# Optimization experiments

Hardware: AMD Instinct MI355X
Metric: run time of the kernel (lower is better)

Reference implementation:

```python
import jax, jax.numpy as jnp
import numpy as np

NUM_HEADS = 16
HEAD_DIM = 64  # d_out // num_heads = 1024 // 16


def setup_inputs() -> dict:
    key = jax.random.key(0)
    ks = jax.random.split(key, 9)
    B, S, D = 2, 2048, 1024
    scale = 0.02
    return {
        "x": jax.random.normal(ks[0], (B, S, D), jnp.float32),
        "Wq": jax.random.normal(ks[1], (D, D), jnp.float32) * scale,
        "bq": jax.random.normal(ks[2], (D,), jnp.float32) * scale,
        "Wk": jax.random.normal(ks[3], (D, D), jnp.float32) * scale,
        "bk": jax.random.normal(ks[4], (D,), jnp.float32) * scale,
        "Wv": jax.random.normal(ks[5], (D, D), jnp.float32) * scale,
        "bv": jax.random.normal(ks[6], (D,), jnp.float32) * scale,
        "Wo": jax.random.normal(ks[7], (D, D), jnp.float32) * scale,
        "bo": jax.random.normal(ks[8], (D,), jnp.float32) * scale,
    }


def reference(x, Wq, bq, Wk, bk, Wv, bv, Wo, bo):
    B, S, D = x.shape
    H, Dh = NUM_HEADS, HEAD_DIM
    # QKV projections (torch Linear: x @ W.T + b; here W stored as [d_in, d_out])
    q = (x @ Wq + bq).reshape(B, S, H, Dh).transpose(0, 2, 1, 3)  # [B,H,S,Dh]
    k = (x @ Wk + bk).reshape(B, S, H, Dh).transpose(0, 2, 1, 3)
    v = (x @ Wv + bv).reshape(B, S, H, Dh).transpose(0, 2, 1, 3)
    scores = jnp.einsum("bhqd,bhkd->bhqk", q, k)
    # causal mask applied before scaling (as in source; -inf unaffected by scale)
    causal = jnp.tril(jnp.ones((S, S), dtype=bool))
    scores = jnp.where(causal, scores, -jnp.inf) / jnp.sqrt(jnp.float32(Dh))
    attn = jax.nn.softmax(scores, axis=-1)  # dropout=0.0 (eval)
    ctx = jnp.einsum("bhqk,bhkd->bhqd", attn, v)  # [B,H,S,Dh]
    ctx = ctx.transpose(0, 2, 1, 3).reshape(B, S, D)
    return ctx @ Wo + bo
```

## Files before the change

### kernel.cpp

```cpp
#include <hip/hip_runtime.h>
#include <math.h>


#define H_  16
#define DH_ 64
#define D_  1024
#define S_  2048
#define B_  2

typedef __attribute__((ext_vector_type(8))) short short8;
typedef __attribute__((ext_vector_type(4))) float f32x4;

__device__ __forceinline__ unsigned short f2bf(float f) {
    union { float f; unsigned int u; } v; v.f = f;
    unsigned int r = (v.u + 0x7fffu + ((v.u >> 16) & 1u)) >> 16;
    return (unsigned short)r;
}

__device__ __forceinline__ void gload_lds16(const void* g, void* l) {
    __builtin_amdgcn_global_load_lds(
        (const __attribute__((address_space(1))) void*)g,
        (__attribute__((address_space(3))) void*)l, 16, 0, 0);
}

__global__ __launch_bounds__(256) void cvt_x_k(const float* __restrict__ x,
                                               unsigned short* __restrict__ xb)
{
    int i = (blockIdx.x * 256 + threadIdx.x) * 8;
    float4 a = *(const float4*)&x[i];
    float4 b = *(const float4*)&x[i + 4];
    uint4 o;
    o.x = f2bf(a.x) | ((unsigned)f2bf(a.y) << 16);
    o.y = f2bf(a.z) | ((unsigned)f2bf(a.w) << 16);
    o.z = f2bf(b.x) | ((unsigned)f2bf(b.y) << 16);
    o.w = f2bf(b.z) | ((unsigned)f2bf(b.w) << 16);
    *(uint4*)&xb[i] = o;
}

__global__ __launch_bounds__(256) void tr_w_k(
    const float* __restrict__ W0, const float* __restrict__ W1,
    const float* __restrict__ W2, const float* __restrict__ W3,
    unsigned short* __restrict__ wt)
{
    const float* W = W0;
    if (blockIdx.z == 1) W = W1; else if (blockIdx.z == 2) W = W2;
    else if (blockIdx.z == 3) W = W3;
    unsigned short* out = wt + (size_t)blockIdx.z * 1048576;

    __shared__ float t[64][65];
    const int k0 = blockIdx.x * 64, n0 = blockIdx.y * 64;
    const int r = threadIdx.x >> 4, c4 = (threadIdx.x & 15) * 4;

    #pragma unroll
    for (int p = 0; p < 4; ++p) {
        float4 v = *(const float4*)&W[(size_t)(k0 + r + 16 * p) * D_ + n0 + c4];
        t[r + 16 * p][c4 + 0] = v.x; t[r + 16 * p][c4 + 1] = v.y;
        t[r + 16 * p][c4 + 2] = v.z; t[r + 16 * p][c4 + 3] = v.w;
    }
    __syncthreads();
    #pragma unroll
    for (int p = 0; p < 4; ++p) {
        int nn = r + 16 * p;
        uint2 o;
        o.x = f2bf(t[c4 + 0][nn]) | ((unsigned)f2bf(t[c4 + 1][nn]) << 16);
        o.y = f2bf(t[c4 + 2][nn]) | ((unsigned)f2bf(t[c4 + 3][nn]) << 16);
        *(uint2*)&out[(size_t)(n0 + nn) * D_ + k0 + c4] = o;
    }
}

template<int QKV>
__global__ __launch_bounds__(256) void gemm_bf16(
    const unsigned short* __restrict__ Ab,
    const unsigned short* __restrict__ Wt,
    const float* __restrict__ b0, const float* __restrict__ b1,
    const float* __restrict__ b2,
    void* __restrict__ o0, void* __restrict__ o1, void* __restrict__ o2)
{
    const unsigned short* W = Wt;
    const float* bias = b0;
    int z = 0;
    if (QKV) {
        z = blockIdx.z;
        W = Wt + (size_t)z * 1048576;
        if (z == 1) bias = b1; else if (z == 2) bias = b2;
    }
    const int n0 = blockIdx.x * 128, j0 = blockIdx.y * 128;
    const int tid = threadIdx.x;
    const int lane = tid & 63;
    const int wq = tid >> 6, wm = wq >> 1, wn = wq & 1;
    const int lr = lane & 15, lk = lane >> 4;

    __shared__ __align__(16) char smem[32768];

    f32x4 acc[4][4] = {};

    for (int k0 = 0; k0 < D_; k0 += 64) {
        __syncthreads();
        #pragma unroll
        for (int c = 0; c < 4; ++c) {
            int u = c * 256 + tid;
            int r = u >> 3, sp = u & 7, sl = sp ^ (r & 7);
            gload_lds16(&Ab[(size_t)(n0 + r) * D_ + k0 + sl * 8], &smem[u * 16]);
        }
        #pragma unroll
        for (int c = 0; c < 4; ++c) {
            int u = c * 256 + tid;
            int r = u >> 3, sp = u & 7, sl = sp ^ (r & 7);
            gload_lds16(&W[(size_t)(j0 + r) * D_ + k0 + sl * 8],
                        &smem[16384 + u * 16]);
        }
        __syncthreads();
        #pragma unroll
        for (int kc = 0; kc < 2; ++kc) {
            short8 a[4], b[4];
            #pragma unroll
            for (int m = 0; m < 4; ++m) {
                int row = wm * 64 + m * 16 + lr;
                int sp = (kc * 4 + lk) ^ (row & 7);
                a[m] = *(const short8*)&smem[row * 128 + sp * 16];
            }
            #pragma unroll
            for (int n = 0; n < 4; ++n) {
                int row = wn * 64 + n * 16 + lr;
                int sp = (kc * 4 + lk) ^ (row & 7);
                b[n] = *(const short8*)&smem[16384 + row * 128 + sp * 16];
            }
            #pragma unroll
            for (int m = 0; m < 4; ++m)
                #pragma unroll
                for (int n = 0; n < 4; ++n)
                    acc[m][n] = __builtin_amdgcn_mfma_f32_16x16x32_bf16(
                        a[m], b[n], acc[m][n], 0, 0, 0);
        }
    }

    float bn[4];
    #pragma unroll
    for (int n = 0; n < 4; ++n) bn[n] = bias[j0 + wn * 64 + n * 16 + lr];

    #pragma unroll
    for (int m = 0; m < 4; ++m) {
        #pragma unroll
        for (int n = 0; n < 4; ++n) {
            int col = j0 + wn * 64 + n * 16 + lr;
            int row0 = n0 + wm * 64 + m * 16 + lk * 4;
            if (QKV) {
                int head = col >> 6, dh = col & 63;
                int bb = row0 >> 11, s0 = row0 & (S_ - 1);
                float v0 = acc[m][n][0] + bn[n], v1 = acc[m][n][1] + bn[n];
                float v2 = acc[m][n][2] + bn[n], v3 = acc[m][n][3] + bn[n];
                if (z < 2) {
                    unsigned short* out = (unsigned short*)(z == 0 ? o0 : o1);
                    size_t base = ((size_t)((bb << 4) + head) * S_) * 64 + dh;
                    out[base + (size_t)(s0 + 0) * 64] = f2bf(v0);
                    out[base + (size_t)(s0 + 1) * 64] = f2bf(v1);
                    out[base + (size_t)(s0 + 2) * 64] = f2bf(v2);
                    out[base + (size_t)(s0 + 3) * 64] = f2bf(v3);
                } else {
                    unsigned short* out = (unsigned short*)o2;
                    uint2 pk;
                    pk.x = f2bf(v0) | ((unsigned)f2bf(v1) << 16);
                    pk.y = f2bf(v2) | ((unsigned)f2bf(v3) << 16);
                    *(uint2*)&out[((size_t)((bb << 4) + head) * 64 + dh) * S_ + s0] = pk;
                }
            } else {
                float* out = (float*)o0;
                #pragma unroll
                for (int r = 0; r < 4; ++r)
                    out[(size_t)(row0 + r) * D_ + col] = acc[m][n][r] + bn[n];
            }
        }
    }
}

__global__ __launch_bounds__(256) void attn_mfma(
    const unsigned short* __restrict__ q, const unsigned short* __restrict__ k,
    const unsigned short* __restrict__ vt, unsigned short* __restrict__ ctx)
{
    const int bh = blockIdx.x;
    const int qt = 31 - blockIdx.y;
    const int tid = threadIdx.x;
    const int lane = tid & 63, wq = tid >> 6;
    const int lx = lane & 15, hi = lane >> 4;

    __shared__ __align__(16) char smem[24576];
    char* Pw = &smem[16384 + wq * 2048];

    short8 qf[2];
    {
        const unsigned short* qrow =
            q + ((size_t)bh * S_ + qt * 64 + wq * 16 + lx) * 64;
        qf[0] = *(const short8*)&qrow[hi * 8];
        qf[1] = *(const short8*)&qrow[32 + hi * 8];
    }

    f32x4 o[4] = {};
    float m = -INFINITY, l = 0.f;
    const int qg = qt * 64 + wq * 16 + lx;

    for (int kt = 0; kt <= qt; ++kt) {
        __syncthreads();
        #pragma unroll
        for (int c = 0; c < 2; ++c) {
            int u = c * 256 + tid;
            int r = u >> 3, sp = u & 7, sl = sp ^ (r & 7);
            gload_lds16(&k[((size_t)bh * S_ + kt * 64 + r) * 64 + sl * 8],
                        &smem[u * 16]);
        }
        #pragma unroll
        for (int c = 0; c < 2; ++c) {
            int u = c * 256 + tid;
            int r = u >> 3, sp = u & 7, sl = sp ^ (r & 7);
            gload_lds16(&vt[((size_t)bh * 64 + r) * S_ + kt * 64 + sl * 8],
                        &smem[8192 + u * 16]);
        }
        __syncthreads();

        f32x4 s[4] = {};
        #pragma unroll
        for (int rt = 0; rt < 4; ++rt) {
            #pragma unroll
            for (int ks = 0; ks < 2; ++ks) {
                int row = rt * 16 + lx;
                int sp = (ks * 4 + hi) ^ (row & 7);
                short8 kf = *(const short8*)&smem[row * 128 + sp * 16];
                s[rt] = __builtin_amdgcn_mfma_f32_16x16x32_bf16(
                    kf, qf[ks], s[rt], 0, 0, 0);
            }
        }

        if (kt == qt) {
            #pragma unroll
            for (int rt = 0; rt < 4; ++rt)
                #pragma unroll
                for (int r = 0; r < 4; ++r) {
                    int kvg = kt * 64 + rt * 16 + hi * 4 + r;
                    s[rt][r] = (kvg > qg) ? -INFINITY : s[rt][r] * 0.125f;
                }
        } else {
            #pragma unroll
            for (int rt = 0; rt < 4; ++rt)
                #pragma unroll
                for (int r = 0; r < 4; ++r) s[rt][r] *= 0.125f;
        }

        float tmax = s[0][0];
        #pragma unroll
        for (int rt = 0; rt < 4; ++rt) {
            tmax = fmaxf(tmax, fmaxf(fmaxf(s[rt][0], s[rt][1]),
                                     fmaxf(s[rt][2], s[rt][3])));
        }
        tmax = fmaxf(tmax, __shfl_xor(tmax, 16));
        tmax = fmaxf(tmax, __shfl_xor(tmax, 32));
        float mn = fmaxf(m, tmax);
        float corr = __expf(m - mn);
        float ps = 0.f;
        #pragma unroll
        for (int rt = 0; rt < 4; ++rt)
            #pragma unroll
            for (int r = 0; r < 4; ++r) {
                s[rt][r] = __expf(s[rt][r] - mn);
                ps += s[rt][r];
            }
        ps += __shfl_xor(ps, 16);
        ps += __shfl_xor(ps, 32);
        l = l * corr + ps;
        m = mn;

        #pragma unroll
        for (int r = 0; r < 4; ++r) {
            float cr = __shfl(corr, hi * 4 + r);
            #pragma unroll
            for (int ct = 0; ct < 4; ++ct) o[ct][r] *= cr;
        }

        #pragma unroll
        for (int rt = 0; rt < 4; ++rt) {
            uint2 pk;
            pk.x = f2bf(s[rt][0]) | ((unsigned)f2bf(s[rt][1]) << 16);
            pk.y = f2bf(s[rt][2]) | ((unsigned)f2bf(s[rt][3]) << 16);
            int sl = 2 * rt + (hi >> 1);
            *(uint2*)&Pw[lx * 128 + ((sl ^ (lx & 7)) * 16) + (hi & 1) * 8] = pk;
        }
        short8 pf[2];
        #pragma unroll
        for (int ks = 0; ks < 2; ++ks) {
            int sl = ks * 4 + hi;
            pf[ks] = *(const short8*)&Pw[lx * 128 + ((sl ^ (lx & 7)) * 16)];
        }

        #pragma unroll
        for (int ct = 0; ct < 4; ++ct) {
            #pragma unroll
            for (int ks = 0; ks < 2; ++ks) {
                int row = ct * 16 + lx;
                int sp = (ks * 4 + hi) ^ (row & 7);
                short8 vf = *(const short8*)&smem[8192 + row * 128 + sp * 16];
                o[ct] = __builtin_amdgcn_mfma_f32_16x16x32_bf16(
                    pf[ks], vf, o[ct], 0, 0, 0);
            }
        }
    }

    const int b = bh >> 4, h = bh & (H_ - 1);
    #pragma unroll
    for (int r = 0; r < 4; ++r) {
        float inv = 1.0f / __shfl(l, hi * 4 + r);
        int srow = qt * 64 + wq * 16 + hi * 4 + r;
        #pragma unroll
        for (int ct = 0; ct < 4; ++ct)
            ctx[((size_t)(b * S_ + srow)) * D_ + h * 64 + ct * 16 + lx] =
                f2bf(o[ct][r] * inv);
    }
}

extern "C" void kernel_launch(void* const* d_in, const int* in_sizes, int n_in,
                              void* d_out, int out_size, void* d_ws, size_t ws_size,
                              hipStream_t stream)
{
    const float* x  = (const float*)d_in[0];
    const float* Wq = (const float*)d_in[1];
    const float* bq = (const float*)d_in[2];
    const float* Wk = (const float*)d_in[3];
    const float* bk = (const float*)d_in[4];
    const float* Wv = (const float*)d_in[5];
    const float* bv = (const float*)d_in[6];
    const float* Wo = (const float*)d_in[7];
    const float* bo = (const float*)d_in[8];
    float* out = (float*)d_out;

    const size_t per = (size_t)B_ * H_ * S_ * DH_;
    unsigned short* qb  = (unsigned short*)d_ws;
    unsigned short* kb  = qb + per;
    unsigned short* vtb = kb + per;
    unsigned short* xb  = vtb + per;
    unsigned short* wt  = xb + per;
    unsigned short* cb  = xb;

    cvt_x_k<<<2048, 256, 0, stream>>>(x, xb);
    tr_w_k<<<dim3(16, 16, 4), 256, 0, stream>>>(Wq, Wk, Wv, Wo, wt);

    gemm_bf16<1><<<dim3(32, 8, 3), 256, 0, stream>>>(
        xb, wt, bq, bk, bv, qb, kb, vtb);

    attn_mfma<<<dim3(32, 32), 256, 0, stream>>>(qb, kb, vtb, cb);

    gemm_bf16<0><<<dim3(32, 8, 1), 256, 0, stream>>>(
        cb, wt + 3u * 1048576u, bo, nullptr, nullptr, out, nullptr, nullptr);
}
```

Baseline: 189.6 us.

## Fold softmax scale into Q, defer rescaling, load K/V directly to registers

The Q projection now carries the 1/sqrt(d)*log2(e) factor, so attention uses exp2 with no per-score multiply. The online softmax skips the max update and accumulator rescale unless the new max exceeds the old by a threshold. K and V fragments are loaded straight from global memory into registers instead of staged through LDS with barriers. The attention grid is remapped so consecutive blocks share heads. The GEMM gains a transposed-MFMA mode that gives vectorized epilogue stores, and the QKV launch is split into a Q/K launch and a V launch. Deferred rescaling risks exp overflow if scores grow past the threshold, and dropping LDS staging means each wave reads K/V from global memory on its own.

Result: slower. 291.4 us (+53.7%).

```diff
diff --git a/kernel.cpp b/kernel.cpp
--- a/kernel.cpp
+++ b/kernel.cpp
@@ -11,10 +11,27 @@
 typedef __attribute__((ext_vector_type(8))) short short8;
 typedef __attribute__((ext_vector_type(4))) float f32x4;
 
+#define QSCALE 0.18033688011112042f
+#define DEFER_THR 11.5416f
+
 __device__ __forceinline__ unsigned short f2bf(float f) {
     union { float f; unsigned int u; } v; v.f = f;
     unsigned int r = (v.u + 0x7fffu + ((v.u >> 16) & 1u)) >> 16;
     return (unsigned short)r;
+}
+
+__device__ __forceinline__ unsigned cvt_pk_bf16(float lo, float hi) {
+    unsigned r;
+    asm("v_cvt_pk_bf16_f32 %0, %1, %2" : "=v"(r) : "v"(lo), "v"(hi));
+    return r;
+}
+
+__device__ __forceinline__ float fast_exp2(float x) {
+#if __has_builtin(__builtin_amdgcn_exp2f)
+    return __builtin_amdgcn_exp2f(x);
+#else
+    return exp2f(x);
+#endif
 }
 
 __device__ __forceinline__ void gload_lds16(const void* g, void* l) {
@@ -68,7 +85,7 @@
     }
 }
 
-template<int QKV>
+template<int QKV, int CT>
 __global__ __launch_bounds__(256) void gemm_bf16(
     const unsigned short* __restrict__ Ab,
     const unsigned short* __restrict__ Wt,
@@ -82,7 +99,7 @@
     if (QKV) {
         z = blockIdx.z;
         W = Wt + (size_t)z * 1048576;
-        if (z == 1) bias = b1; else if (z == 2) bias = b2;
+        if (z == 1) bias = b1;
     }
     const int n0 = blockIdx.x * 128, j0 = blockIdx.y * 128;
     const int tid = threadIdx.x;
@@ -128,46 +145,70 @@
             #pragma unroll
             for (int m = 0; m < 4; ++m)
                 #pragma unroll
-                for (int n = 0; n < 4; ++n)
-                    acc[m][n] = __builtin_amdgcn_mfma_f32_16x16x32_bf16(
-                        a[m], b[n], acc[m][n], 0, 0, 0);
-        }
-    }
-
-    float bn[4];
-    #pragma unroll
-    for (int n = 0; n < 4; ++n) bn[n] = bias[j0 + wn * 64 + n * 16 + lr];
-
-    #pragma unroll
-    for (int m = 0; m < 4; ++m) {
+                for (int n = 0; n < 4; ++n) {
+                    if (CT)
+                        acc[m][n] = __builtin_amdgcn_mfma_f32_16x16x32_bf16(
+                            b[n], a[m], acc[m][n], 0, 0, 0);
+                    else
+                        acc[m][n] = __builtin_amdgcn_mfma_f32_16x16x32_bf16(
+                            a[m], b[n], acc[m][n], 0, 0, 0);
+                }
+        }
+    }
+
+    if (QKV && CT) {
+        const float sc = (z == 0) ? QSCALE : 1.0f;
+        unsigned short* out = (unsigned short*)(z == 0 ? o0 : o1);
         #pragma unroll
         for (int n = 0; n < 4; ++n) {
-            int col = j0 + wn * 64 + n * 16 + lr;
-            int row0 = n0 + wm * 64 + m * 16 + lk * 4;
-            if (QKV) {
+            int f0 = j0 + wn * 64 + n * 16 + lk * 4;
+            int head = f0 >> 6, dh0 = f0 & 63;
+            float4 b4 = *(const float4*)&bias[f0];
+            #pragma unroll
+            for (int m = 0; m < 4; ++m) {
+                int tok = n0 + wm * 64 + m * 16 + lr;
+                int bb = tok >> 11, s = tok & (S_ - 1);
+                uint2 pk;
+                pk.x = f2bf((acc[m][n][0] + b4.x) * sc)
+                     | ((unsigned)f2bf((acc[m][n][1] + b4.y) * sc) << 16);
+                pk.y = f2bf((acc[m][n][2] + b4.z) * sc)
+                     | ((unsigned)f2bf((acc[m][n][3] + b4.w) * sc) << 16);
+                *(uint2*)&out[(((size_t)(bb * H_ + head)) * S_ + s) * 64 + dh0] = pk;
+            }
+        }
+    } else if (QKV) {
+        unsigned short* out = (unsigned short*)o0;
+        float bn[4];
+        #pragma unroll
+        for (int n = 0; n < 4; ++n) bn[n] = bias[j0 + wn * 64 + n * 16 + lr];
+        #pragma unroll
+        for (int m = 0; m < 4; ++m) {
+            #pragma unroll
+            for (int n = 0; n < 4; ++n) {
+                int col = j0 + wn * 64 + n * 16 + lr;
+                int row0 = n0 + wm * 64 + m * 16 + lk * 4;
                 int head = col >> 6, dh = col & 63;
                 int bb = row0 >> 11, s0 = row0 & (S_ - 1);
-                float v0 = acc[m][n][0] + bn[n], v1 = acc[m][n][1] + bn[n];
-                float v2 = acc[m][n][2] + bn[n], v3 = acc[m][n][3] + bn[n];
-                if (z < 2) {
-                    unsigned short* out = (unsigned short*)(z == 0 ? o0 : o1);
-                    size_t base = ((size_t)((bb << 4) + head) * S_) * 64 + dh;
-                    out[base + (size_t)(s0 + 0) * 64] = f2bf(v0);
-                    out[base + (size_t)(s0 + 1) * 64] = f2bf(v1);
-                    out[base + (size_t)(s0 + 2) * 64] = f2bf(v2);
-                    out[base + (size_t)(s0 + 3) * 64] = f2bf(v3);
-                } else {
-                    unsigned short* out = (unsigned short*)o2;
-                    uint2 pk;
-                    pk.x = f2bf(v0) | ((unsigned)f2bf(v1) << 16);
-                    pk.y = f2bf(v2) | ((unsigned)f2bf(v3) << 16);
-                    *(uint2*)&out[((size_t)((bb << 4) + head) * 64 + dh) * S_ + s0] = pk;
-                }
-            } else {
-                float* out = (float*)o0;
-                #pragma unroll
-                for (int r = 0; r < 4; ++r)
-                    out[(size_t)(row0 + r) * D_ + col] = acc[m][n][r] + bn[n];
+                uint2 pk;
+                pk.x = f2bf(acc[m][n][0] + bn[n])
+                     | ((unsigned)f2bf(acc[m][n][1] + bn[n]) << 16);
+                pk.y = f2bf(acc[m][n][2] + bn[n])
+                     | ((unsigned)f2bf(acc[m][n][3] + bn[n]) << 16);
+                *(uint2*)&out[((size_t)((bb << 4) + head) * 64 + dh) * S_ + s0] = pk;
+            }
+        }
+    } else {
+        float* out = (float*)o0;
+        #pragma unroll
+        for (int n = 0; n < 4; ++n) {
+            int f0 = j0 + wn * 64 + n * 16 + lk * 4;
+            float4 b4 = *(const float4*)&bias[f0];
+            #pragma unroll
+            for (int m = 0; m < 4; ++m) {
+                int tok = n0 + wm * 64 + m * 16 + lr;
+                float4 ov = { acc[m][n][0] + b4.x, acc[m][n][1] + b4.y,
+                              acc[m][n][2] + b4.z, acc[m][n][3] + b4.w };
+                *(float4*)&out[(size_t)tok * D_ + f0] = ov;
             }
         }
     }
@@ -177,108 +218,116 @@
     const unsigned short* __restrict__ q, const unsigned short* __restrict__ k,
     const unsigned short* __restrict__ vt, unsigned short* __restrict__ ctx)
 {
-    const int bh = blockIdx.x;
-    const int qt = 31 - blockIdx.y;
+    const int i = blockIdx.x;
+    const int c = i & 7, rr = i >> 3;
+    const int bh = c * 4 + (rr & 3);
+    const int yt = 31 - (rr >> 2);
     const int tid = threadIdx.x;
     const int lane = tid & 63, wq = tid >> 6;
     const int lx = lane & 15, hi = lane >> 4;
 
-    __shared__ __align__(16) char smem[24576];
-    char* Pw = &smem[16384 + wq * 2048];
+    __shared__ __align__(16) char Pall[8192];
+    char* Pw = Pall + wq * 2048;
+
+    const int b = bh >> 4, h = bh & (H_ - 1);
+    const int qbase = yt * 64 + wq * 16;
+    const int nkt = yt + 1;
+
+    const unsigned short* Kb = k + (size_t)bh * S_ * 64;
+    const unsigned short* Vb = vt + (size_t)bh * 64 * S_;
 
     short8 qf[2];
     {
-        const unsigned short* qrow =
-            q + ((size_t)bh * S_ + qt * 64 + wq * 16 + lx) * 64;
+        const unsigned short* qrow = q + ((size_t)bh * S_ + qbase + lx) * 64;
         qf[0] = *(const short8*)&qrow[hi * 8];
         qf[1] = *(const short8*)&qrow[32 + hi * 8];
     }
 
     f32x4 o[4] = {};
     float m = -INFINITY, l = 0.f;
-    const int qg = qt * 64 + wq * 16 + lx;
-
-    for (int kt = 0; kt <= qt; ++kt) {
-        __syncthreads();
-        #pragma unroll
-        for (int c = 0; c < 2; ++c) {
-            int u = c * 256 + tid;
-            int r = u >> 3, sp = u & 7, sl = sp ^ (r & 7);
-            gload_lds16(&k[((size_t)bh * S_ + kt * 64 + r) * 64 + sl * 8],
-                        &smem[u * 16]);
-        }
-        #pragma unroll
-        for (int c = 0; c < 2; ++c) {
-            int u = c * 256 + tid;
-            int r = u >> 3, sp = u & 7, sl = sp ^ (r & 7);
-            gload_lds16(&vt[((size_t)bh * 64 + r) * S_ + kt * 64 + sl * 8],
-                        &smem[8192 + u * 16]);
-        }
-        __syncthreads();
+    const int qg = qbase + lx;
+
+    for (int kt = 0; kt < nkt; ++kt) {
+        short8 kf[4][2], vf[4][2];
+        #pragma unroll
+        for (int rt = 0; rt < 4; ++rt)
+            #pragma unroll
+            for (int ks = 0; ks < 2; ++ks)
+                kf[rt][ks] = *(const short8*)
+                    &Kb[(size_t)(kt * 64 + rt * 16 + lx) * 64 + ks * 32 + hi * 8];
+        #pragma unroll
+        for (int ct = 0; ct < 4; ++ct)
+            #pragma unroll
+            for (int ks = 0; ks < 2; ++ks)
+                vf[ct][ks] = *(const short8*)
+                    &Vb[(size_t)(ct * 16 + lx) * S_ + kt * 64 + ks * 32 + hi * 8];
 
         f32x4 s[4] = {};
         #pragma unroll
-        for (int rt = 0; rt < 4; ++rt) {
-            #pragma unroll
-            for (int ks = 0; ks < 2; ++ks) {
-                int row = rt * 16 + lx;
-                int sp = (ks * 4 + hi) ^ (row & 7);
-                short8 kf = *(const short8*)&smem[row * 128 + sp * 16];
+        for (int rt = 0; rt < 4; ++rt)
+            #pragma unroll
+            for (int ks = 0; ks < 2; ++ks)
                 s[rt] = __builtin_amdgcn_mfma_f32_16x16x32_bf16(
-                    kf, qf[ks], s[rt], 0, 0, 0);
-            }
-        }
-
-        if (kt == qt) {
+                    kf[rt][ks], qf[ks], s[rt], 0, 0, 0);
+
+        if (kt == nkt - 1) {
             #pragma unroll
             for (int rt = 0; rt < 4; ++rt)
                 #pragma unroll
                 for (int r = 0; r < 4; ++r) {
                     int kvg = kt * 64 + rt * 16 + hi * 4 + r;
-                    s[rt][r] = (kvg > qg) ? -INFINITY : s[rt][r] * 0.125f;
+                    if (kvg > qg) s[rt][r] = -INFINITY;
                 }
-        } else {
-            #pragma unroll
-            for (int rt = 0; rt < 4; ++rt)
-                #pragma unroll
-                for (int r = 0; r < 4; ++r) s[rt][r] *= 0.125f;
         }
 
         float tmax = s[0][0];
         #pragma unroll
-        for (int rt = 0; rt < 4; ++rt) {
+        for (int rt = 0; rt < 4; ++rt)
             tmax = fmaxf(tmax, fmaxf(fmaxf(s[rt][0], s[rt][1]),
                                      fmaxf(s[rt][2], s[rt][3])));
-        }
         tmax = fmaxf(tmax, __shfl_xor(tmax, 16));
         tmax = fmaxf(tmax, __shfl_xor(tmax, 32));
-        float mn = fmaxf(m, tmax);
-        float corr = __expf(m - mn);
-        float ps = 0.f;
-        #pragma unroll
-        for (int rt = 0; rt < 4; ++rt)
+
+        if (__any(tmax > m + DEFER_THR)) {
+            float mn = fmaxf(m, tmax);
+            float corr = fast_exp2(m - mn);
+            m = mn;
+            float ps = 0.f;
+            #pragma unroll
+            for (int rt = 0; rt < 4; ++rt)
+                #pragma unroll
+                for (int r = 0; r < 4; ++r) {
+                    s[rt][r] = fast_exp2(s[rt][r] - mn);
+                    ps += s[rt][r];
+                }
+            ps += __shfl_xor(ps, 16);
+            ps += __shfl_xor(ps, 32);
+            l = l * corr + ps;
             #pragma unroll
             for (int r = 0; r < 4; ++r) {
-                s[rt][r] = __expf(s[rt][r] - mn);
-                ps += s[rt][r];
-            }
-        ps += __shfl_xor(ps, 16);
-        ps += __shfl_xor(ps, 32);
-        l = l * corr + ps;
-        m = mn;
-
-        #pragma unroll
-        for (int r = 0; r < 4; ++r) {
-            float cr = __shfl(corr, hi * 4 + r);
-            #pragma unroll
-            for (int ct = 0; ct < 4; ++ct) o[ct][r] *= cr;
+                float cr = __shfl(corr, hi * 4 + r);
+                #pragma unroll
+                for (int ct = 0; ct < 4; ++ct) o[ct][r] *= cr;
+            }
+        } else {
+            float ps = 0.f;
+            #pragma unroll
+            for (int rt = 0; rt < 4; ++rt)
+                #pragma unroll
+                for (int r = 0; r < 4; ++r) {
+                    s[rt][r] = fast_exp2(s[rt][r] - m);
+                    ps += s[rt][r];
+                }
+            ps += __shfl_xor(ps, 16);
+            ps += __shfl_xor(ps, 32);
+            l += ps;
         }
 
         #pragma unroll
         for (int rt = 0; rt < 4; ++rt) {
             uint2 pk;
-            pk.x = f2bf(s[rt][0]) | ((unsigned)f2bf(s[rt][1]) << 16);
-            pk.y = f2bf(s[rt][2]) | ((unsigned)f2bf(s[rt][3]) << 16);
+            pk.x = cvt_pk_bf16(s[rt][0], s[rt][1]);
+            pk.y = cvt_pk_bf16(s[rt][2], s[rt][3]);
             int sl = 2 * rt + (hi >> 1);
             *(uint2*)&Pw[lx * 128 + ((sl ^ (lx & 7)) * 16) + (hi & 1) * 8] = pk;
         }
@@ -290,23 +339,17 @@
         }
 
         #pragma unroll
-        for (int ct = 0; ct < 4; ++ct) {
-            #pragma unroll
-            for (int ks = 0; ks < 2; ++ks) {
-                int row = ct * 16 + lx;
-                int sp = (ks * 4 + hi) ^ (row & 7);
-                short8 vf = *(const short8*)&smem[8192 + row * 128 + sp * 16];
+        for (int ct = 0; ct < 4; ++ct)
+            #pragma unroll
+            for (int ks = 0; ks < 2; ++ks)
                 o[ct] = __builtin_amdgcn_mfma_f32_16x16x32_bf16(
-                    pf[ks], vf, o[ct], 0, 0, 0);
-            }
-        }
-    }
-
-    const int b = bh >> 4, h = bh & (H_ - 1);
+                    pf[ks], vf[ct][ks], o[ct], 0, 0, 0);
+    }
+
     #pragma unroll
     for (int r = 0; r < 4; ++r) {
         float inv = 1.0f / __shfl(l, hi * 4 + r);
-        int srow = qt * 64 + wq * 16 + hi * 4 + r;
+        int srow = qbase + hi * 4 + r;
         #pragma unroll
         for (int ct = 0; ct < 4; ++ct)
             ctx[((size_t)(b * S_ + srow)) * D_ + h * 64 + ct * 16 + lx] =
@@ -340,11 +383,13 @@
     cvt_x_k<<<2048, 256, 0, stream>>>(x, xb);
     tr_w_k<<<dim3(16, 16, 4), 256, 0, stream>>>(Wq, Wk, Wv, Wo, wt);
 
-    gemm_bf16<1><<<dim3(32, 8, 3), 256, 0, stream>>>(
-        xb, wt, bq, bk, bv, qb, kb, vtb);
-
-    attn_mfma<<<dim3(32, 32), 256, 0, stream>>>(qb, kb, vtb, cb);
-
-    gemm_bf16<0><<<dim3(32, 8, 1), 256, 0, stream>>>(
+    gemm_bf16<1, 1><<<dim3(32, 8, 2), 256, 0, stream>>>(
+        xb, wt, bq, bk, nullptr, qb, kb, nullptr);
+    gemm_bf16<1, 0><<<dim3(32, 8, 1), 256, 0, stream>>>(
+        xb, wt + 2u * 1048576u, bv, nullptr, nullptr, vtb, nullptr, nullptr);
+
+    attn_mfma<<<1024, 256, 0, stream>>>(qb, kb, vtb, cb);
+
+    gemm_bf16<0, 1><<<dim3(32, 8, 1), 256, 0, stream>>>(
         cb, wt + 3u * 1048576u, bo, nullptr, nullptr, out, nullptr, nullptr);
 }
```
